# Optimization experiments

Hardware: AMD Instinct MI355X
Metric: run time of the kernel (lower is better)

The kernel has to match this reference:

```python
import jax, jax.numpy as jnp
import numpy as np

N_PATCH, N_Z, K, BS = 16, 128, 10, 1024
D = N_PATCH * N_Z


def setup_inputs() -> dict:
    key = jax.random.key(0)
    k1, k2, k3, k4 = jax.random.split(key, 4)
    z = jax.random.normal(k1, (BS, D), dtype=jnp.float32)
    m = jax.random.normal(k2, (K, D), dtype=jnp.float32)
    L = jax.random.normal(k3, (K, D, D), dtype=jnp.float32)
    components = jax.random.randint(k4, (BS,), 0, K, dtype=jnp.int64)
    return {"z": z, "m": m, "L": L, "components": components}


def reference(z, m, L, components):
    # samps[k] = m[k] + z @ L[k].T   -> (K, BS, D)
    samps = jnp.einsum('bd,ked->kbe', z, L) + m[:, None, :]
    # one-hot mask-and-sum over components == gather selected expert per sample
    x = samps[components, jnp.arange(z.shape[0])]  # (BS, D)
    return x.reshape(-1, N_PATCH, N_Z)
```

## Files before the change

kernel.cpp:

```cpp
#include <hip/hip_runtime.h>
#include <hip/hip_bf16.h>


#define DDIM  2048
#define BSAMP 1024
#define KCOMP 10
#define MPAD  160
#define NT    32
#define BK    32
#define NITER (DDIM / BK)
#define ABYTES (MPAD * BK * 2)
#define BBYTES (NT * BK * 4)
#define STAGE_BYTES (ABYTES + BBYTES)

typedef __attribute__((ext_vector_type(8))) short bf16x8;
typedef __attribute__((ext_vector_type(4))) float f32x4;

__device__ __forceinline__ void async16(void* lds, const void* g) {
    __builtin_amdgcn_global_load_lds(
        (const __attribute__((address_space(1))) void*)g,
        (__attribute__((address_space(3))) void*)lds, 16, 0, 0);
}

__device__ __forceinline__ short bfs(float x) {
    __hip_bfloat16 h = __float2bfloat16(x);
    return *reinterpret_cast<short*>(&h);
}

__global__ void build_map(const int* __restrict__ comp,
                          int* __restrict__ rowmap,
                          int* __restrict__ counts) {
    __shared__ int sc[KCOMP];
    const int t = threadIdx.x;
    if (t < KCOMP) sc[t] = 0;
    __syncthreads();
    const int c = comp[t];
    const int r = atomicAdd(&sc[c], 1);
    if (r < MPAD) rowmap[c * MPAD + r] = t;
    __syncthreads();
    if (t < KCOMP) counts[t] = sc[t];
}

__global__ void zgather(const float* __restrict__ z,
                        const int* __restrict__ rowmap,
                        short* __restrict__ zb) {
    const int ks  = blockIdx.x;
    const int t   = threadIdx.x;
    const int src = rowmap[ks] & (BSAMP - 1);
    const float* zr = z + (size_t)src * DDIM + t * 8;
    f32x4 x = *(const f32x4*)zr;
    f32x4 y = *(const f32x4*)(zr + 4);
    bf16x8 r;
#pragma unroll
    for (int i = 0; i < 4; ++i) { r[i] = bfs(x[i]); r[4 + i] = bfs(y[i]); }
    *(bf16x8*)(zb + (size_t)ks * DDIM + t * 8) = r;
}

__global__ __launch_bounds__(256, 4)
void gmm_gemm(const short* __restrict__ zb,
              const float* __restrict__ mvec,
              const float* __restrict__ Lmat,
              const int* __restrict__ rowmap,
              const int* __restrict__ counts,
              float* __restrict__ out) {
    __shared__ __attribute__((aligned(16))) char smem[2 * STAGE_BYTES];
    const int t    = threadIdx.x;
    const int lane = t & 63;
    const int w    = t >> 6;
    const int mh   = w >> 1;
    const int nh   = w & 1;
    const int k    = blockIdx.y;
    const int n0   = blockIdx.x * NT;
    const float* Lk = Lmat + (size_t)k * DDIM * DDIM;
    const short* zk = zb + (size_t)k * MPAD * DDIM;
    const int cnt  = counts[k];

    int mtmax = (cnt - mh * 80 + 15) >> 4;
    mtmax = mtmax < 0 ? 0 : (mtmax > 5 ? 5 : mtmax);

    const int ar0 = t >> 2,         ac0 = (((t & 3) - (ar0 >> 1)) & 3) * 8;
    const int ar1 = 64 + (t >> 2),  ac1 = (((t & 3) - (ar1 >> 1)) & 3) * 8;
    const int ar2 = 128 + (t >> 2), ac2 = (((t & 3) - (ar2 >> 1)) & 3) * 8;
    const int br = t >> 3,          bc = ((t & 7) ^ (br & 7)) * 4;
    const unsigned ub = (unsigned)(t & ~63) * 16;

    auto stage = [&](int buf, int it) {
        char* lb = smem + buf * STAGE_BYTES;
        const int d0 = it * BK;
        async16(lb + ub,        zk + (size_t)ar0 * DDIM + d0 + ac0);
        async16(lb + 4096 + ub, zk + (size_t)ar1 * DDIM + d0 + ac1);
        if (t < 128)
            async16(lb + 8192 + ub, zk + (size_t)ar2 * DDIM + d0 + ac2);
        async16(lb + ABYTES + ub, Lk + (size_t)(n0 + br) * DDIM + d0 + bc);
    };

    f32x4 acc[5];
#pragma unroll
    for (int mt = 0; mt < 5; ++mt) acc[mt] = (f32x4){0.f, 0.f, 0.f, 0.f};

    stage(0, 0);
    __syncthreads();

    const int fr = lane & 15;
    const int g  = lane >> 4;
    const int rb = nh * 16 + fr;
    const int h0 = ((2 * g)     ^ (rb & 7)) * 4;
    const int h1 = ((2 * g + 1) ^ (rb & 7)) * 4;

    for (int it = 0; it < NITER; ++it) {
        if (it + 1 < NITER) stage((it + 1) & 1, it + 1);
        const char* lb = smem + (it & 1) * STAGE_BYTES;
        const short* A = (const short*)lb;
        const float* B = (const float*)(lb + ABYTES);

        f32x4 x = *(const f32x4*)(B + rb * 32 + h0);
        f32x4 y = *(const f32x4*)(B + rb * 32 + h1);
        bf16x8 bb;
#pragma unroll
        for (int i = 0; i < 4; ++i) { bb[i] = bfs(x[i]); bb[4 + i] = bfs(y[i]); }

#pragma unroll
        for (int mt = 0; mt < 5; ++mt) {
            if (mt < mtmax) {
                const int ra = mh * 80 + mt * 16 + fr;
                const int gs = ((g + (ra >> 1)) & 3) * 8;
                bf16x8 a = *(const bf16x8*)(A + ra * 32 + gs);
                acc[mt] = __builtin_amdgcn_mfma_f32_16x16x32_bf16(a, bb, acc[mt], 0, 0, 0);
            }
        }
        __syncthreads();
    }

    const int rquad = g * 4;
    const int e  = n0 + nh * 16 + fr;
    const float mu = mvec[k * DDIM + e];
#pragma unroll
    for (int mt = 0; mt < 5; ++mt) {
        if (mt < mtmax) {
            const int sb = mh * 80 + mt * 16 + rquad;
#pragma unroll
            for (int r = 0; r < 4; ++r) {
                const int slot = sb + r;
                if (slot < cnt) {
                    const int b = rowmap[k * MPAD + slot];
                    out[(size_t)b * DDIM + e] = acc[mt][r] + mu;
                }
            }
        }
    }
}

extern "C" void kernel_launch(void* const* d_in, const int* in_sizes, int n_in,
                              void* d_out, int out_size, void* d_ws, size_t ws_size,
                              hipStream_t stream) {
    const float* z    = (const float*)d_in[0];
    const float* mvec = (const float*)d_in[1];
    const float* Lmat = (const float*)d_in[2];
    const int* comp   = (const int*)d_in[3];
    float* out        = (float*)d_out;

    int* rowmap = (int*)d_ws;
    int* counts = rowmap + KCOMP * MPAD;
    short* zb   = (short*)((char*)d_ws + 8192);

    build_map<<<1, BSAMP, 0, stream>>>(comp, rowmap, counts);
    zgather<<<KCOMP * MPAD, 256, 0, stream>>>(z, rowmap, zb);
    gmm_gemm<<<dim3(DDIM / NT, KCOMP), 256, 0, stream>>>(zb, mvec, Lmat,
                                                         rowmap, counts, out);
}
```

Baseline: 284.7 us.

## Pre-tile gathered z into contiguous swizzled per-k-step tiles for linear async loads

The gather kernel now writes bf16 z rows directly in the per-iteration LDS tile layout (160x32 tiles, pre-swizzled), so each GEMM stage copies one contiguous 10KB block with linear 16-byte async loads instead of strided row reads. The LDS A-fragment address simplifies to a constant base plus mt offset. This is meant to cut address arithmetic and scattered global traffic for the A operand, and it relies on the new swizzle matching between producer and consumer.

```diff
diff --git a/kernel.cpp b/kernel.cpp
--- a/kernel.cpp
+++ b/kernel.cpp
@@ -9,7 +9,8 @@
 #define NT    32
 #define BK    32
 #define NITER (DDIM / BK)
-#define ABYTES (MPAD * BK * 2)
+#define TILEB (MPAD * BK * 2)
+#define ABYTES TILEB
 #define BBYTES (NT * BK * 4)
 #define STAGE_BYTES (ABYTES + BBYTES)
 
@@ -44,16 +45,27 @@
 __global__ void zgather(const float* __restrict__ z,
                         const int* __restrict__ rowmap,
                         short* __restrict__ zb) {
-    const int ks  = blockIdx.x;
-    const int t   = threadIdx.x;
-    const int src = rowmap[ks] & (BSAMP - 1);
-    const float* zr = z + (size_t)src * DDIM + t * 8;
-    f32x4 x = *(const f32x4*)zr;
-    f32x4 y = *(const f32x4*)(zr + 4);
-    bf16x8 r;
+    const int k  = blockIdx.x;
+    const int sp = blockIdx.y;
+    const int t  = threadIdx.x;
+    const int c  = t & 7;
+    const int g  = c & 3;
+    const int s0 = rowmap[k * MPAD + 2 * sp]     & (BSAMP - 1);
+    const int s1 = rowmap[k * MPAD + 2 * sp + 1] & (BSAMP - 1);
+    const int src = (c >> 2) ? s1 : s0;
+    const int swz = (c ^ (sp & 7)) * 16;
+    char* kbase = (char*)zb + (size_t)k * NITER * TILEB + sp * 128 + swz;
 #pragma unroll
-    for (int i = 0; i < 4; ++i) { r[i] = bfs(x[i]); r[4 + i] = bfs(y[i]); }
-    *(bf16x8*)(zb + (size_t)ks * DDIM + t * 8) = r;
+    for (int p = 0; p < 2; ++p) {
+        const int it = p * 32 + (t >> 3);
+        const float* zr = z + (size_t)src * DDIM + it * BK + g * 8;
+        f32x4 x = *(const f32x4*)zr;
+        f32x4 y = *(const f32x4*)(zr + 4);
+        bf16x8 r;
+#pragma unroll
+        for (int i = 0; i < 4; ++i) { r[i] = bfs(x[i]); r[4 + i] = bfs(y[i]); }
+        *(bf16x8*)(kbase + (size_t)it * TILEB) = r;
+    }
 }
 
 __global__ __launch_bounds__(256, 4)
@@ -72,26 +84,24 @@
     const int k    = blockIdx.y;
     const int n0   = blockIdx.x * NT;
     const float* Lk = Lmat + (size_t)k * DDIM * DDIM;
-    const short* zk = zb + (size_t)k * MPAD * DDIM;
+    const char* zt  = (const char*)zb + (size_t)k * NITER * TILEB;
     const int cnt  = counts[k];
 
     int mtmax = (cnt - mh * 80 + 15) >> 4;
     mtmax = mtmax < 0 ? 0 : (mtmax > 5 ? 5 : mtmax);
 
-    const int ar0 = t >> 2,         ac0 = (((t & 3) - (ar0 >> 1)) & 3) * 8;
-    const int ar1 = 64 + (t >> 2),  ac1 = (((t & 3) - (ar1 >> 1)) & 3) * 8;
-    const int ar2 = 128 + (t >> 2), ac2 = (((t & 3) - (ar2 >> 1)) & 3) * 8;
     const int br = t >> 3,          bc = ((t & 7) ^ (br & 7)) * 4;
     const unsigned ub = (unsigned)(t & ~63) * 16;
 
     auto stage = [&](int buf, int it) {
         char* lb = smem + buf * STAGE_BYTES;
-        const int d0 = it * BK;
-        async16(lb + ub,        zk + (size_t)ar0 * DDIM + d0 + ac0);
-        async16(lb + 4096 + ub, zk + (size_t)ar1 * DDIM + d0 + ac1);
+        const char* at = zt + (size_t)it * TILEB;
+        async16(lb + ub,        at + t * 16);
+        async16(lb + 4096 + ub, at + 4096 + t * 16);
         if (t < 128)
-            async16(lb + 8192 + ub, zk + (size_t)ar2 * DDIM + d0 + ac2);
-        async16(lb + ABYTES + ub, Lk + (size_t)(n0 + br) * DDIM + d0 + bc);
+            async16(lb + 8192 + ub, at + 8192 + t * 16);
+        async16(lb + ABYTES + ub,
+                Lk + (size_t)(n0 + br) * DDIM + it * BK + bc);
     };
 
     f32x4 acc[5];
@@ -106,11 +116,13 @@
     const int rb = nh * 16 + fr;
     const int h0 = ((2 * g)     ^ (rb & 7)) * 4;
     const int h1 = ((2 * g + 1) ^ (rb & 7)) * 4;
+    const int frh = fr >> 1;
+    const int fra = (fr & 1) * 4 + g;
+    const int abase = (mh * 40 + frh) * 128 + ((fra ^ frh) * 16);
 
     for (int it = 0; it < NITER; ++it) {
         if (it + 1 < NITER) stage((it + 1) & 1, it + 1);
         const char* lb = smem + (it & 1) * STAGE_BYTES;
-        const short* A = (const short*)lb;
         const float* B = (const float*)(lb + ABYTES);
 
         f32x4 x = *(const f32x4*)(B + rb * 32 + h0);
@@ -122,9 +134,7 @@
 #pragma unroll
         for (int mt = 0; mt < 5; ++mt) {
             if (mt < mtmax) {
-                const int ra = mh * 80 + mt * 16 + fr;
-                const int gs = ((g + (ra >> 1)) & 3) * 8;
-                bf16x8 a = *(const bf16x8*)(A + ra * 32 + gs);
+                bf16x8 a = *(const bf16x8*)(lb + abase + mt * 1024);
                 acc[mt] = __builtin_amdgcn_mfma_f32_16x16x32_bf16(a, bb, acc[mt], 0, 0, 0);
             }
         }
@@ -164,7 +174,7 @@
     short* zb   = (short*)((char*)d_ws + 8192);
 
     build_map<<<1, BSAMP, 0, stream>>>(comp, rowmap, counts);
-    zgather<<<KCOMP * MPAD, 256, 0, stream>>>(z, rowmap, zb);
+    zgather<<<dim3(KCOMP, MPAD / 2), 256, 0, stream>>>(z, rowmap, zb);
     gmm_gemm<<<dim3(DDIM / NT, KCOMP), 256, 0, stream>>>(zb, mvec, Lmat,
                                                          rowmap, counts, out);
 }
```

Result: faster. 269.5 us (-5.3%).
